# Kernel optimization log

Measured on AMD Instinct MI355X. Metric: run time of the kernel, lower is better.

## Reference

```python
import jax, jax.numpy as jnp
import numpy as np

T_VID = 129  # TACoS iou grid size

def make_iou_mask_map():
    m = np.zeros((129, 129), np.float32)
    for i in range(0, 128):
        m[i, 1 + i:min(i + 17, 129)] = 1.0
    for i in range(0, 128 - 16, 2):
        m[i, list(range(18 + i, min(33 + i, 129), 2))] = 1.0
    for i in range(0, 128 - 32, 4):
        m[i, list(range(36 + i, min(65 + i, 129), 4))] = 1.0
    for i in range(0, 128 - 64, 8):
        m[i, list(range(72 + i, 129, 8))] = 1.0
    return jnp.asarray(m)

def setup_inputs() -> dict:
    key = jax.random.key(0)
    B, L, T, D, CH, V = 8, 100, T_VID, 512, 512, 1000
    ks = jax.random.split(key, 20)
    g = lambda k, shp, fan: jax.random.normal(k, shp, jnp.float32) * (1.0 / np.sqrt(fan))
    return {
        'hidden_states_text': jax.random.normal(ks[0], (B, L, D), jnp.float32),
        'hidden_states_object': jax.random.normal(ks[1], (B, T, D), jnp.float32),
        # final_mlp (text head): D->CH->V
        'w_t1': g(ks[2], (D, CH), D), 'b_t1': jnp.zeros((CH,), jnp.float32),
        'w_t2': g(ks[3], (CH, V), CH), 'b_t2': jnp.zeros((V,), jnp.float32),
        # final_mlp_2: D -> 3D (+ReLU)
        'w2': g(ks[4], (D, 3 * D), D), 'b2': jnp.zeros((3 * D,), jnp.float32),
        # final_mlp_3: 3D -> CH -> 3
        'w3a': g(ks[5], (3 * D, CH), 3 * D), 'b3a': jnp.zeros((CH,), jnp.float32),
        'w3b': g(ks[6], (CH, 3), CH), 'b3b': jnp.zeros((3,), jnp.float32),
        # final_mlp_s/e/c: D -> CH -> 1
        'w_s1': g(ks[7], (D, CH), D), 'b_s1': jnp.zeros((CH,), jnp.float32),
        'w_s2': g(ks[8], (CH, 1), CH), 'b_s2': jnp.zeros((1,), jnp.float32),
        'w_e1': g(ks[9], (D, CH), D), 'b_e1': jnp.zeros((CH,), jnp.float32),
        'w_e2': g(ks[10], (CH, 1), CH), 'b_e2': jnp.zeros((1,), jnp.float32),
        'w_c1': g(ks[11], (D, CH), D), 'b_c1': jnp.zeros((CH,), jnp.float32),
        'w_c2': g(ks[12], (CH, 1), CH), 'b_c2': jnp.zeros((1,), jnp.float32),
    }

def _head(x, w1, b1, w2, b2):
    return jax.nn.relu(x @ w1 + b1) @ w2 + b2

def reference(hidden_states_text, hidden_states_object,
              w_t1, b_t1, w_t2, b_t2, w2, b2, w3a, b3a, w3b, b3b,
              w_s1, b_s1, w_s2, b_s2, w_e1, b_e1, w_e2, b_e2,
              w_c1, b_c1, w_c2, b_c2):
    D = hidden_states_object.shape[-1]
    T = hidden_states_object.shape[1]
    # text head (dropout is identity at inference)
    logits_text = _head(hidden_states_text, w_t1, b_t1, w_t2, b_t2)
    # final_mlp_2 then split into start/center/end streams, each [B,T,D]
    h = jax.nn.relu(hidden_states_object @ w2 + b2)
    hs, hc, he = h[..., :D], h[..., D:2 * D], h[..., 2 * D:]
    # final_mlp_3 first linear decomposed over the concat blocks:
    # grid[b,i,j] = W_s.hs[i] + W_c.hc[(i+j)//2] + W_e.he[j] + b  (same math as
    # cat(repeat(hs), gather(hc), repeat(he)) @ w3a, without the 3D grid)
    ps = hc @ w3a[D:2 * D]            # [B,T,CH] (center projection, gathered below)
    pS = hs @ w3a[:D]                 # [B,T,CH]
    pE = he @ w3a[2 * D:]             # [B,T,CH]
    idx = (jnp.arange(T)[:, None] + jnp.arange(T)[None, :]) // 2  # [T,T] center index
    grid = pS[:, :, None, :] + ps[:, idx, :] + pE[:, None, :, :] + b3a  # [B,T,T,CH]
    logits_iou = (jax.nn.relu(grid) @ w3b + b3b)  # [B,T,T,3]
    logits_iou = jnp.transpose(logits_iou, (0, 3, 1, 2))  # [B,3,T,T]
    logits_visual = jnp.concatenate([
        _head(hs, w_s1, b_s1, w_s2, b_s2),
        _head(he, w_e1, b_e1, w_e2, b_e2),
        _head(hc, w_c1, b_c1, w_c2, b_c2)], axis=-1)  # [B,T,3]
    return logits_text, logits_visual, logits_iou, make_iou_mask_map()
```

## Files before the change

### kernel.cpp

```cpp
#include <hip/hip_runtime.h>
#include <hip/hip_bf16.h>

typedef unsigned short ushort_t;
typedef __attribute__((ext_vector_type(8))) unsigned short u16x8;
typedef __attribute__((ext_vector_type(8))) short bf16x8;
typedef __attribute__((ext_vector_type(4))) float f32x4;

constexpr int BB = 8, LL = 100, TT = 129, DD = 512, CH = 512, VV = 1000;
constexpr int M_TXT = BB * LL;
constexpr int M_OBJ = BB * TT;
constexpr int P_SLAB = M_OBJ * DD;
constexpr int N_IOU = BB * 3 * TT * TT;
constexpr int N_VIS = 3 * M_OBJ;
constexpr int N_MASK = TT * TT;

constexpr int OUT_TEXT = 0;
constexpr int OUT_VIS  = M_TXT * VV;
constexpr int OUT_IOU  = OUT_VIS + N_VIS;
constexpr int OUT_MASK = OUT_IOU + N_IOU;

constexpr size_t WB_TEXT = 0;
constexpr size_t WB_OBJ  = WB_TEXT + 819200;
constexpr size_t WB_WT1  = WB_OBJ  + 1056768;
constexpr size_t WB_WT2  = WB_WT1  + 524288;
constexpr size_t WB_W2T  = WB_WT2  + 1024000;
constexpr size_t WB_W3AT = WB_W2T  + 1572864;
constexpr size_t WB_WS1T = WB_W3AT + 1572864;
constexpr size_t WB_WE1T = WB_WS1T + 524288;
constexpr size_t WB_WC1T = WB_WE1T + 524288;
constexpr size_t WB_T1   = WB_WC1T + 524288;
constexpr size_t WB_H    = WB_T1   + 819200;
constexpr size_t WB_P    = WB_H    + 3170304;

__device__ __forceinline__ ushort_t f2bf(float x) {
    __hip_bfloat16 h = __float2bfloat16(x);
    return *(ushort_t*)&h;
}

struct TDesc { const float* src; ushort_t* dst; int R, C, tiles, ctiles; };
struct PrepArgs {
    const float* act_a; ushort_t* act_da; int na4;
    const float* act_b; ushort_t* act_db; int nb4;
    int nact_blocks;
    TDesc t[7];
};

__global__ __launch_bounds__(256)
void prep_kernel(PrepArgs pa)
{
    const int bxg = blockIdx.x;
    if (bxg < pa.nact_blocks) {
        int gid = bxg * 256 + threadIdx.x;
        const float* src; ushort_t* dst;
        if (gid < pa.na4) { src = pa.act_a + gid * 4; dst = pa.act_da + gid * 4; }
        else { gid -= pa.na4; if (gid >= pa.nb4) return; src = pa.act_b + gid * 4; dst = pa.act_db + gid * 4; }
        f32x4 v = *(const f32x4*)src;
        dst[0] = f2bf(v[0]); dst[1] = f2bf(v[1]); dst[2] = f2bf(v[2]); dst[3] = f2bf(v[3]);
        return;
    }
    __shared__ float tl[32][65];
    int bx = bxg - pa.nact_blocks;
    TDesc e;
    #pragma unroll
    for (int i = 0; i < 7; ++i) {
        e = pa.t[i];
        if (bx < e.tiles) break;
        bx -= e.tiles;
    }
    const int t = threadIdx.x;
    const int rt = bx / e.ctiles, ct = bx - rt * e.ctiles;
    {
        const int c = t & 63, ty = t >> 6;
        const int gc = ct * 64 + c;
        const bool cok = gc < e.C;
        const float* sp = e.src + (size_t)(rt * 32) * e.C + gc;
        #pragma unroll
        for (int i = 0; i < 8; ++i) {
            const int rr = ty + i * 4;
            tl[rr][c] = cok ? sp[(size_t)rr * e.C] : 0.0f;
        }
    }
    __syncthreads();
    {
        const int dr = t >> 2, dc0 = (t & 3) << 3;
        const int gdr = ct * 64 + dr;
        if (gdr < e.C) {
            u16x8 v;
            #pragma unroll
            for (int u = 0; u < 8; ++u) v[u] = f2bf(tl[dc0 + u][dr]);
            *(u16x8*)&e.dst[(size_t)gdr * e.R + rt * 32 + dc0] = v;
        }
    }
}

struct GemmDesc {
    const ushort_t* A; int lda;
    const ushort_t* Bt; int ldb;
    const float* bias;
    void* C; int ldc;
    int M, N, K;
    int mode;
    const float* w2head;
    float* vbase;
    int vhead;
    int ntiles, ntx;
};
struct MegaArgs {
    GemmDesc d[7];
    int gemm_blocks;
    const float *b3b, *bs2, *be2, *bc2;
    float* out;
};

__global__ __launch_bounds__(256)
void mega_kernel(MegaArgs args)
{
    extern __shared__ char smem[];
    if ((int)blockIdx.x >= args.gemm_blocks) {
        int g = (blockIdx.x - args.gemm_blocks) * 1024 + threadIdx.x * 4;
        #pragma unroll
        for (int u = 0; u < 4; ++u, ++g) {
            int gg = g;
            if (gg < N_IOU) {
                const int bk = gg / (TT * TT);
                const int k = bk - (bk / 3) * 3;
                args.out[OUT_IOU + gg] = args.b3b[k];
                continue;
            }
            gg -= N_IOU;
            if (gg < N_VIS) {
                const int head = gg - (gg / 3) * 3;
                const float bias = head == 0 ? args.bs2[0] : (head == 1 ? args.be2[0] : args.bc2[0]);
                args.out[OUT_VIS + gg] = bias;
                continue;
            }
            gg -= N_VIS;
            if (gg < N_MASK) {
                const int i = gg / TT, j = gg - i * TT;
                const int d = j - i;
                bool v = false;
                if (i < 128 && d >= 1 && d <= 16) v = true;
                if (!v && (i & 1) == 0 && i <= 110 && d >= 18 && d <= 32 && (d & 1) == 0) v = true;
                if (!v && (i & 3) == 0 && i <= 92  && d >= 36 && d <= 64 && (d & 3) == 0) v = true;
                if (!v && (i & 7) == 0 && i <= 56  && d >= 72 && (d & 7) == 0) v = true;
                args.out[OUT_MASK + gg] = v ? 1.0f : 0.0f;
            }
        }
        return;
    }

    int bx = blockIdx.x, zi = 0;
    while (bx >= args.d[zi].ntiles) { bx -= args.d[zi].ntiles; ++zi; }
    const GemmDesc g = args.d[zi];
    const int tyT = bx / g.ntx, txT = bx - tyT * g.ntx;
    const int m0 = tyT * 128, n0 = txT * 128;

    ushort_t* ldsA = (ushort_t*)smem;
    ushort_t* ldsB = (ushort_t*)smem + 16384;

    const int tid = threadIdx.x;
    const int w = tid >> 6, l = tid & 63;
    const int wr = w >> 1, wc = w & 1;

    const int srow = l >> 2;
    const int scol = (l & 3) << 3;
    const int wbase = w << 4;

    f32x4 acc[4][4];
    #pragma unroll
    for (int mi = 0; mi < 4; ++mi)
        #pragma unroll
        for (int ni = 0; ni < 4; ++ni)
            acc[mi][ni] = f32x4{0.f, 0.f, 0.f, 0.f};

    const int nk = g.K >> 6;

    auto stage = [&](int buf, int k0) {
        #pragma unroll
        for (int ks = 0; ks < 2; ++ks) {
            const int sb = ((buf * 2 + ks) << 12);
            #pragma unroll
            for (int q = 0; q < 2; ++q) {
                int gm = m0 + (q << 6) + wbase + srow; if (gm >= g.M) gm = g.M - 1;
                __builtin_amdgcn_global_load_lds(
                    (const __attribute__((address_space(1))) unsigned int*)(g.A + (size_t)gm * g.lda + k0 + (ks << 5) + scol),
                    (__attribute__((address_space(3))) unsigned int*)(ldsA + sb + (((q << 6) + wbase) << 5)),
                    16, 0, 0);
                int gn = n0 + (q << 6) + wbase + srow; if (gn >= g.N) gn = g.N - 1;
                __builtin_amdgcn_global_load_lds(
                    (const __attribute__((address_space(1))) unsigned int*)(g.Bt + (size_t)gn * g.ldb + k0 + (ks << 5) + scol),
                    (__attribute__((address_space(3))) unsigned int*)(ldsB + sb + (((q << 6) + wbase) << 5)),
                    16, 0, 0);
            }
        }
    };

    stage(0, 0);
    int cur = 0;
    const int fr = l & 15, kq = (l >> 4) << 3;

    for (int kt = 0; kt < nk; ++kt) {
        __syncthreads();
        if (kt + 1 < nk) stage(cur ^ 1, (kt + 1) << 6);
        #pragma unroll
        for (int ks = 0; ks < 2; ++ks) {
            const int sb = ((cur * 2 + ks) << 12);
            bf16x8 av[4], bv[4];
            #pragma unroll
            for (int mi = 0; mi < 4; ++mi)
                av[mi] = *(const bf16x8*)(ldsA + sb + ((((wr << 6) + (mi << 4) + fr) << 5) + kq));
            #pragma unroll
            for (int ni = 0; ni < 4; ++ni)
                bv[ni] = *(const bf16x8*)(ldsB + sb + ((((wc << 6) + (ni << 4) + fr) << 5) + kq));
            #pragma unroll
            for (int mi = 0; mi < 4; ++mi)
                #pragma unroll
                for (int ni = 0; ni < 4; ++ni)
                    acc[mi][ni] = __builtin_amdgcn_mfma_f32_16x16x32_bf16(av[mi], bv[ni], acc[mi][ni], 0, 0, 0);
        }
        cur ^= 1;
    }

    const int rq = (l >> 4) << 2;
    if (g.mode == 2) {
        float s[4][4];
        #pragma unroll
        for (int mi = 0; mi < 4; ++mi)
            #pragma unroll
            for (int r = 0; r < 4; ++r) s[mi][r] = 0.f;
        #pragma unroll
        for (int ni = 0; ni < 4; ++ni) {
            const int col = n0 + (wc << 6) + (ni << 4) + fr;
            const float bb = g.bias[col];
            const float wv = g.w2head[col];
            #pragma unroll
            for (int mi = 0; mi < 4; ++mi)
                #pragma unroll
                for (int r = 0; r < 4; ++r) {
                    float v = fmaxf(acc[mi][ni][r] + bb, 0.f);
                    s[mi][r] = fmaf(v, wv, s[mi][r]);
                }
        }
        #pragma unroll
        for (int off = 1; off < 16; off <<= 1)
            #pragma unroll
            for (int mi = 0; mi < 4; ++mi)
                #pragma unroll
                for (int r = 0; r < 4; ++r)
                    s[mi][r] += __shfl_xor(s[mi][r], off);
        if (fr == 0) {
            #pragma unroll
            for (int mi = 0; mi < 4; ++mi)
                #pragma unroll
                for (int r = 0; r < 4; ++r) {
                    const int row = m0 + (wr << 6) + (mi << 4) + rq + r;
                    if (row < g.M) atomicAdd(&g.vbase[row * 3 + g.vhead], s[mi][r]);
                }
        }
    } else {
        #pragma unroll
        for (int ni = 0; ni < 4; ++ni) {
            const int col = n0 + (wc << 6) + (ni << 4) + fr;
            const float bb = (g.bias && col < g.N) ? g.bias[col] : 0.f;
            #pragma unroll
            for (int mi = 0; mi < 4; ++mi)
                #pragma unroll
                for (int r = 0; r < 4; ++r) {
                    const int row = m0 + (wr << 6) + (mi << 4) + rq + r;
                    if (row < g.M && col < g.N) {
                        float v = acc[mi][ni][r] + bb;
                        if (g.mode == 1) {
                            v = fmaxf(v, 0.f);
                            ((ushort_t*)g.C)[(size_t)row * g.ldc + col] = f2bf(v);
                        } else {
                            ((float*)g.C)[(size_t)row * g.ldc + col] = v;
                        }
                    }
                }
        }
    }
}

__global__ __launch_bounds__(256)
void iou_kernel(const float* __restrict__ P, const float* __restrict__ w3b,
                float* __restrict__ out)
{
    __shared__ __align__(16) float sP[96 * 132];
    __shared__ __align__(16) float sW[768];

    const int tid = threadIdx.x;
    const int b = blockIdx.z >> 1;
    const int half = blockIdx.z & 1;
    const int i0 = blockIdx.y * 32, j0 = blockIdx.x * 32;
    const int idx0 = (i0 + j0) >> 1;
    const int par = (i0 + j0) & 1;

    for (int f = tid; f < 768; f += 256) {
        const int ph = f / 384;
        const int rem = f - ph * 384;
        const int k = rem >> 7, c = rem & 127;
        sW[f] = w3b[((half << 8) + (ph << 7) + c) * 3 + k];
    }

    const int ii = tid >> 4, jj = tid & 15;
    const int o = ((ii + jj + par) >> 1) + 32;

    const f32x4 z4 = {0.f, 0.f, 0.f, 0.f};
    f32x4 av00[3], av01[3], av10[3], av11[3];
    #pragma unroll
    for (int k = 0; k < 3; ++k) { av00[k] = z4; av01[k] = z4; av10[k] = z4; av11[k] = z4; }

    for (int ph = 0; ph < 2; ++ph) {
        const int c0 = (half << 8) + (ph << 7);
        if (ph) __syncthreads();
        for (int f = tid; f < 3072; f += 256) {
            const int row = f >> 5;
            const int pos = (f & 31) << 2;
            const int a = row >> 5;
            const int r = row & 31;
            int rg = (a == 0) ? (i0 + r) : (a == 1) ? (idx0 + r) : (j0 + r);
            if (rg > 128) rg = 128;
            f32x4 v = *(const f32x4*)&P[(size_t)a * P_SLAB + ((size_t)(b * TT) + rg) * DD + c0 + pos];
            *(f32x4*)&sP[row * 132 + pos] = v;
        }
        __syncthreads();

        const float* rs0 = &sP[ii * 132];
        const float* rs1 = &sP[(ii + 16) * 132];
        const float* rp0 = &sP[o * 132];
        const float* rp1 = &sP[(o + 8) * 132];
        const float* rp2 = &sP[(o + 16) * 132];
        const float* re0 = &sP[(64 + jj) * 132];
        const float* re1 = &sP[(64 + jj + 16) * 132];
        const float* swp = &sW[ph * 384];

        #pragma unroll 2
        for (int c = 0; c < 128; c += 4) {
            const f32x4 s0 = *(const f32x4*)&rs0[c];
            const f32x4 s1 = *(const f32x4*)&rs1[c];
            const f32x4 p0 = *(const f32x4*)&rp0[c];
            const f32x4 p1 = *(const f32x4*)&rp1[c];
            const f32x4 p2 = *(const f32x4*)&rp2[c];
            const f32x4 e0 = *(const f32x4*)&re0[c];
            const f32x4 e1 = *(const f32x4*)&re1[c];
            const f32x4 w0 = *(const f32x4*)&swp[c];
            const f32x4 w1 = *(const f32x4*)&swp[128 + c];
            const f32x4 w2 = *(const f32x4*)&swp[256 + c];

            const f32x4 t00 = s0 + e0, t01 = s0 + e1, t10 = s1 + e0, t11 = s1 + e1;
            const f32x4 v00 = __builtin_elementwise_max(t00 + p0, z4);
            const f32x4 v01 = __builtin_elementwise_max(t01 + p1, z4);
            const f32x4 v10 = __builtin_elementwise_max(t10 + p1, z4);
            const f32x4 v11 = __builtin_elementwise_max(t11 + p2, z4);

            av00[0] = __builtin_elementwise_fma(v00, w0, av00[0]);
            av00[1] = __builtin_elementwise_fma(v00, w1, av00[1]);
            av00[2] = __builtin_elementwise_fma(v00, w2, av00[2]);
            av01[0] = __builtin_elementwise_fma(v01, w0, av01[0]);
            av01[1] = __builtin_elementwise_fma(v01, w1, av01[1]);
            av01[2] = __builtin_elementwise_fma(v01, w2, av01[2]);
            av10[0] = __builtin_elementwise_fma(v10, w0, av10[0]);
            av10[1] = __builtin_elementwise_fma(v10, w1, av10[1]);
            av10[2] = __builtin_elementwise_fma(v10, w2, av10[2]);
            av11[0] = __builtin_elementwise_fma(v11, w0, av11[0]);
            av11[1] = __builtin_elementwise_fma(v11, w1, av11[1]);
            av11[2] = __builtin_elementwise_fma(v11, w2, av11[2]);
        }
    }

    auto emit = [&](const f32x4* acc, int i, int j) {
        if (i <= 128 && j <= 128) {
            #pragma unroll
            for (int k = 0; k < 3; ++k) {
                const float s = acc[k][0] + acc[k][1] + acc[k][2] + acc[k][3];
                atomicAdd(&out[OUT_IOU + ((size_t)(b * 3 + k) * TT + i) * TT + j], s);
            }
        }
    };
    emit(av00, i0 + ii, j0 + jj);
    emit(av01, i0 + ii, j0 + jj + 16);
    emit(av10, i0 + ii + 16, j0 + jj);
    emit(av11, i0 + ii + 16, j0 + jj + 16);
}

extern "C" void kernel_launch(void* const* d_in, const int* in_sizes, int n_in,
                              void* d_out, int out_size, void* d_ws, size_t ws_size,
                              hipStream_t stream)
{
    const float* text = (const float*)d_in[0];
    const float* obj  = (const float*)d_in[1];
    const float* w_t1 = (const float*)d_in[2];
    const float* b_t1 = (const float*)d_in[3];
    const float* w_t2 = (const float*)d_in[4];
    const float* b_t2 = (const float*)d_in[5];
    const float* w2   = (const float*)d_in[6];
    const float* b2   = (const float*)d_in[7];
    const float* w3a  = (const float*)d_in[8];
    const float* b3a  = (const float*)d_in[9];
    const float* w3b  = (const float*)d_in[10];
    const float* b3b  = (const float*)d_in[11];
    const float* w_s1 = (const float*)d_in[12];
    const float* b_s1 = (const float*)d_in[13];
    const float* w_s2 = (const float*)d_in[14];
    const float* b_s2 = (const float*)d_in[15];
    const float* w_e1 = (const float*)d_in[16];
    const float* b_e1 = (const float*)d_in[17];
    const float* w_e2 = (const float*)d_in[18];
    const float* b_e2 = (const float*)d_in[19];
    const float* w_c1 = (const float*)d_in[20];
    const float* b_c1 = (const float*)d_in[21];
    const float* w_c2 = (const float*)d_in[22];
    const float* b_c2 = (const float*)d_in[23];

    float* out = (float*)d_out;
    char* ws = (char*)d_ws;
    ushort_t* text_bf = (ushort_t*)(ws + WB_TEXT);
    ushort_t* obj_bf  = (ushort_t*)(ws + WB_OBJ);
    ushort_t* wt1     = (ushort_t*)(ws + WB_WT1);
    ushort_t* wt2     = (ushort_t*)(ws + WB_WT2);
    ushort_t* w2t     = (ushort_t*)(ws + WB_W2T);
    ushort_t* w3at    = (ushort_t*)(ws + WB_W3AT);
    ushort_t* ws1t    = (ushort_t*)(ws + WB_WS1T);
    ushort_t* we1t    = (ushort_t*)(ws + WB_WE1T);
    ushort_t* wc1t    = (ushort_t*)(ws + WB_WC1T);
    ushort_t* T1      = (ushort_t*)(ws + WB_T1);
    ushort_t* H       = (ushort_t*)(ws + WB_H);
    float*    P       = (float*)(ws + WB_P);

    {
        PrepArgs pa;
        pa.act_a = text; pa.act_da = text_bf; pa.na4 = (M_TXT * DD) / 4;
        pa.act_b = obj;  pa.act_db = obj_bf;  pa.nb4 = (M_OBJ * DD) / 4;
        pa.nact_blocks = (pa.na4 + pa.nb4 + 255) / 256;
        pa.t[0] = {w_t1, wt1, 512, 512, 128, 8};
        pa.t[1] = {w_t2, wt2, 512, 1000, 256, 16};
        pa.t[2] = {w2, w2t, 512, 1536, 384, 24};
        pa.t[3] = {w3a, w3at, 1536, 512, 384, 8};
        pa.t[4] = {w_s1, ws1t, 512, 512, 128, 8};
        pa.t[5] = {w_e1, we1t, 512, 512, 128, 8};
        pa.t[6] = {w_c1, wc1t, 512, 512, 128, 8};
        prep_kernel<<<dim3(pa.nact_blocks + 1536), dim3(256), 0, stream>>>(pa);
    }
    {
        MegaArgs a{};
        a.d[0] = {text_bf, DD, wt1, DD, b_t1, T1, CH, M_TXT, CH, DD, 1, nullptr, nullptr, 0, 28, 4};
        a.d[1] = {obj_bf, DD, w2t, DD, b2, H, 3 * DD, M_OBJ, 3 * DD, DD, 1, nullptr, nullptr, 0, 108, 12};
        a.gemm_blocks = 136;
        a.b3b = b3b; a.bs2 = b_s2; a.be2 = b_e2; a.bc2 = b_c2; a.out = out;
        const int ninit = (N_IOU + N_VIS + N_MASK + 1023) / 1024;
        mega_kernel<<<dim3(136 + ninit), dim3(256), 65536, stream>>>(a);
    }
    {
        MegaArgs a{};
        a.d[0] = {T1, CH, wt2, CH, b_t2, out + OUT_TEXT, VV, M_TXT, VV, CH, 0, nullptr, nullptr, 0, 56, 8};
        a.d[1] = {H + 0 * DD, 3 * DD, w3at + 0 * DD, 3 * DD, b3a, P + 0 * P_SLAB, DD, M_OBJ, DD, DD, 0, nullptr, nullptr, 0, 36, 4};
        a.d[2] = {H + 1 * DD, 3 * DD, w3at + 1 * DD, 3 * DD, nullptr, P + 1 * P_SLAB, DD, M_OBJ, DD, DD, 0, nullptr, nullptr, 0, 36, 4};
        a.d[3] = {H + 2 * DD, 3 * DD, w3at + 2 * DD, 3 * DD, nullptr, P + 2 * P_SLAB, DD, M_OBJ, DD, DD, 0, nullptr, nullptr, 0, 36, 4};
        a.d[4] = {H + 0 * DD, 3 * DD, ws1t, DD, b_s1, nullptr, 0, M_OBJ, CH, DD, 2, w_s2, out + OUT_VIS, 0, 36, 4};
        a.d[5] = {H + 2 * DD, 3 * DD, we1t, DD, b_e1, nullptr, 0, M_OBJ, CH, DD, 2, w_e2, out + OUT_VIS, 1, 36, 4};
        a.d[6] = {H + 1 * DD, 3 * DD, wc1t, DD, b_c1, nullptr, 0, M_OBJ, CH, DD, 2, w_c2, out + OUT_VIS, 2, 36, 4};
        a.gemm_blocks = 272;
        a.b3b = b3b; a.bs2 = b_s2; a.be2 = b_e2; a.bc2 = b_c2; a.out = out;
        mega_kernel<<<dim3(272), dim3(256), 65536, stream>>>(a);
    }
    iou_kernel<<<dim3(5, 5, 16), dim3(256), 0, stream>>>(P, w3b, out);
}
```

Before: 76.96 us.

## Defer weight transposes into GEMM kernel and split IoU grid edge handling

Five weight transposes that the first GEMM stage does not need move out of the prep kernel and run as extra blocks of the first mega kernel, overlapping with the text and object GEMMs. The prep kernel therefore finishes sooner. The IoU kernel switches from a 5x5 tile grid, which wasted most of its last row and column of tiles on a single valid index, to 4x4 full tiles plus dedicated edge blocks that compute row 128 and column 128 with per-thread dot products. The bounds checks and clamping disappear from the main tiles, at the cost of a separate, less efficient edge path and more blocks in the first mega kernel.

```diff
diff --git a/kernel.cpp b/kernel.cpp
--- a/kernel.cpp
+++ b/kernel.cpp
@@ -13,6 +13,7 @@
 constexpr int N_IOU = BB * 3 * TT * TT;
 constexpr int N_VIS = 3 * M_OBJ;
 constexpr int N_MASK = TT * TT;
+constexpr int N_EDGE = BB * 257;
 
 constexpr int OUT_TEXT = 0;
 constexpr int OUT_VIS  = M_TXT * VV;
@@ -38,11 +39,39 @@
 }
 
 struct TDesc { const float* src; ushort_t* dst; int R, C, tiles, ctiles; };
+
+__device__ __forceinline__ void do_transpose_tile(const TDesc& e, int bx, int tid, float* tl )
+{
+    const int rt = bx / e.ctiles, ct = bx - rt * e.ctiles;
+    {
+        const int c = tid & 63, ty = tid >> 6;
+        const int gc = ct * 64 + c;
+        const bool cok = gc < e.C;
+        const float* sp = e.src + (size_t)(rt * 32) * e.C + gc;
+        #pragma unroll
+        for (int i = 0; i < 8; ++i) {
+            const int rr = ty + i * 4;
+            tl[rr * 65 + c] = cok ? sp[(size_t)rr * e.C] : 0.0f;
+        }
+    }
+    __syncthreads();
+    {
+        const int dr = tid >> 2, dc0 = (tid & 3) << 3;
+        const int gdr = ct * 64 + dr;
+        if (gdr < e.C) {
+            u16x8 v;
+            #pragma unroll
+            for (int u = 0; u < 8; ++u) v[u] = f2bf(tl[(dc0 + u) * 65 + dr]);
+            *(u16x8*)&e.dst[(size_t)gdr * e.R + rt * 32 + dc0] = v;
+        }
+    }
+}
+
 struct PrepArgs {
     const float* act_a; ushort_t* act_da; int na4;
     const float* act_b; ushort_t* act_db; int nb4;
     int nact_blocks;
-    TDesc t[7];
+    TDesc t[2];
 };
 
 __global__ __launch_bounds__(256)
@@ -58,39 +87,11 @@
         dst[0] = f2bf(v[0]); dst[1] = f2bf(v[1]); dst[2] = f2bf(v[2]); dst[3] = f2bf(v[3]);
         return;
     }
-    __shared__ float tl[32][65];
+    __shared__ float tl[32 * 65];
     int bx = bxg - pa.nact_blocks;
-    TDesc e;
-    #pragma unroll
-    for (int i = 0; i < 7; ++i) {
-        e = pa.t[i];
-        if (bx < e.tiles) break;
-        bx -= e.tiles;
-    }
-    const int t = threadIdx.x;
-    const int rt = bx / e.ctiles, ct = bx - rt * e.ctiles;
-    {
-        const int c = t & 63, ty = t >> 6;
-        const int gc = ct * 64 + c;
-        const bool cok = gc < e.C;
-        const float* sp = e.src + (size_t)(rt * 32) * e.C + gc;
-        #pragma unroll
-        for (int i = 0; i < 8; ++i) {
-            const int rr = ty + i * 4;
-            tl[rr][c] = cok ? sp[(size_t)rr * e.C] : 0.0f;
-        }
-    }
-    __syncthreads();
-    {
-        const int dr = t >> 2, dc0 = (t & 3) << 3;
-        const int gdr = ct * 64 + dr;
-        if (gdr < e.C) {
-            u16x8 v;
-            #pragma unroll
-            for (int u = 0; u < 8; ++u) v[u] = f2bf(tl[dc0 + u][dr]);
-            *(u16x8*)&e.dst[(size_t)gdr * e.R + rt * 32 + dc0] = v;
-        }
-    }
+    TDesc e = pa.t[0];
+    if (bx >= e.tiles) { bx -= e.tiles; e = pa.t[1]; }
+    do_transpose_tile(e, bx, threadIdx.x, tl);
 }
 
 struct GemmDesc {
@@ -108,6 +109,8 @@
 struct MegaArgs {
     GemmDesc d[7];
     int gemm_blocks;
+    TDesc t[5];
+    int wt_blocks;
     const float *b3b, *bs2, *be2, *bc2;
     float* out;
 };
@@ -117,7 +120,19 @@
 {
     extern __shared__ char smem[];
     if ((int)blockIdx.x >= args.gemm_blocks) {
-        int g = (blockIdx.x - args.gemm_blocks) * 1024 + threadIdx.x * 4;
+        int wx = blockIdx.x - args.gemm_blocks;
+        if (wx < args.wt_blocks) {
+            TDesc e;
+            #pragma unroll
+            for (int i = 0; i < 5; ++i) {
+                e = args.t[i];
+                if (wx < e.tiles) break;
+                wx -= e.tiles;
+            }
+            do_transpose_tile(e, wx, threadIdx.x, (float*)smem);
+            return;
+        }
+        int g = (wx - args.wt_blocks) * 1024 + threadIdx.x * 4;
         #pragma unroll
         for (int u = 0; u < 4; ++u, ++g) {
             int gg = g;
@@ -289,11 +304,54 @@
     __shared__ __align__(16) float sW[768];
 
     const int tid = threadIdx.x;
-    const int b = blockIdx.z >> 1;
-    const int half = blockIdx.z & 1;
-    const int i0 = blockIdx.y * 32, j0 = blockIdx.x * 32;
+    const int bxg = blockIdx.x;
+
+    if (bxg >= 256) {
+        for (int f = tid; f < 1536; f += 256) {
+            const int k = f >> 9, c = f & 511;
+            sP[f] = w3b[c * 3 + k];
+        }
+        __syncthreads();
+        const int pt = (bxg - 256) * 64 + (tid >> 2);
+        if (pt >= N_EDGE) return;
+        const int b = pt / 257;
+        const int r = pt - b * 257;
+        int i, j;
+        if (r < 129) { i = 128; j = r; } else { i = r - 129; j = 128; }
+        const int idx = (i + j) >> 1;
+        const int c0 = (tid & 3) << 7;
+
+        const float* rs = P + ((size_t)(b * TT) + i) * DD + c0;
+        const float* rp = P + (size_t)P_SLAB + ((size_t)(b * TT) + idx) * DD + c0;
+        const float* re = P + (size_t)2 * P_SLAB + ((size_t)(b * TT) + j) * DD + c0;
+        const float* w0 = &sP[c0], *w1 = &sP[512 + c0], *w2 = &sP[1024 + c0];
+
+        float a0 = 0.f, a1 = 0.f, a2 = 0.f;
+        for (int c = 0; c < 128; c += 4) {
+            const f32x4 s = *(const f32x4*)&rs[c];
+            const f32x4 p = *(const f32x4*)&rp[c];
+            const f32x4 e = *(const f32x4*)&re[c];
+            #pragma unroll
+            for (int u = 0; u < 4; ++u) {
+                const float v = fmaxf(s[u] + p[u] + e[u], 0.f);
+                a0 = fmaf(v, w0[c + u], a0);
+                a1 = fmaf(v, w1[c + u], a1);
+                a2 = fmaf(v, w2[c + u], a2);
+            }
+        }
+        const size_t base = ((size_t)(b * 3) * TT + i) * TT + j;
+        atomicAdd(&out[OUT_IOU + base], a0);
+        atomicAdd(&out[OUT_IOU + base + TT * TT], a1);
+        atomicAdd(&out[OUT_IOU + base + 2 * TT * TT], a2);
+        return;
+    }
+
+    const int half = bxg & 1;
+    const int b = (bxg >> 1) & 7;
+    const int tj = (bxg >> 4) & 3;
+    const int ti = (bxg >> 6) & 3;
+    const int i0 = ti * 32, j0 = tj * 32;
     const int idx0 = (i0 + j0) >> 1;
-    const int par = (i0 + j0) & 1;
 
     for (int f = tid; f < 768; f += 256) {
         const int ph = f / 384;
@@ -303,7 +361,7 @@
     }
 
     const int ii = tid >> 4, jj = tid & 15;
-    const int o = ((ii + jj + par) >> 1) + 32;
+    const int o = ((ii + jj) >> 1) + 32;
 
     const f32x4 z4 = {0.f, 0.f, 0.f, 0.f};
     f32x4 av00[3], av01[3], av10[3], av11[3];
@@ -317,9 +375,8 @@
             const int row = f >> 5;
             const int pos = (f & 31) << 2;
             const int a = row >> 5;
-            const int r = row & 31;
-            int rg = (a == 0) ? (i0 + r) : (a == 1) ? (idx0 + r) : (j0 + r);
-            if (rg > 128) rg = 128;
+            const int rr = row & 31;
+            const int rg = (a == 0) ? (i0 + rr) : (a == 1) ? (idx0 + rr) : (j0 + rr);
             f32x4 v = *(const f32x4*)&P[(size_t)a * P_SLAB + ((size_t)(b * TT) + rg) * DD + c0 + pos];
             *(f32x4*)&sP[row * 132 + pos] = v;
         }
@@ -369,12 +426,10 @@
     }
 
     auto emit = [&](const f32x4* acc, int i, int j) {
-        if (i <= 128 && j <= 128) {
-            #pragma unroll
-            for (int k = 0; k < 3; ++k) {
-                const float s = acc[k][0] + acc[k][1] + acc[k][2] + acc[k][3];
-                atomicAdd(&out[OUT_IOU + ((size_t)(b * 3 + k) * TT + i) * TT + j], s);
-            }
+        #pragma unroll
+        for (int k = 0; k < 3; ++k) {
+            const float s = acc[k][0] + acc[k][1] + acc[k][2] + acc[k][3];
+            atomicAdd(&out[OUT_IOU + ((size_t)(b * 3 + k) * TT + i) * TT + j], s);
         }
     };
     emit(av00, i0 + ii, j0 + jj);
@@ -433,22 +488,23 @@
         pa.act_b = obj;  pa.act_db = obj_bf;  pa.nb4 = (M_OBJ * DD) / 4;
         pa.nact_blocks = (pa.na4 + pa.nb4 + 255) / 256;
         pa.t[0] = {w_t1, wt1, 512, 512, 128, 8};
-        pa.t[1] = {w_t2, wt2, 512, 1000, 256, 16};
-        pa.t[2] = {w2, w2t, 512, 1536, 384, 24};
-        pa.t[3] = {w3a, w3at, 1536, 512, 384, 8};
-        pa.t[4] = {w_s1, ws1t, 512, 512, 128, 8};
-        pa.t[5] = {w_e1, we1t, 512, 512, 128, 8};
-        pa.t[6] = {w_c1, wc1t, 512, 512, 128, 8};
-        prep_kernel<<<dim3(pa.nact_blocks + 1536), dim3(256), 0, stream>>>(pa);
+        pa.t[1] = {w2, w2t, 512, 1536, 384, 24};
+        prep_kernel<<<dim3(pa.nact_blocks + 512), dim3(256), 0, stream>>>(pa);
     }
     {
         MegaArgs a{};
         a.d[0] = {text_bf, DD, wt1, DD, b_t1, T1, CH, M_TXT, CH, DD, 1, nullptr, nullptr, 0, 28, 4};
         a.d[1] = {obj_bf, DD, w2t, DD, b2, H, 3 * DD, M_OBJ, 3 * DD, DD, 1, nullptr, nullptr, 0, 108, 12};
         a.gemm_blocks = 136;
+        a.t[0] = {w_t2, wt2, 512, 1000, 256, 16};
+        a.t[1] = {w3a, w3at, 1536, 512, 384, 8};
+        a.t[2] = {w_s1, ws1t, 512, 512, 128, 8};
+        a.t[3] = {w_e1, we1t, 512, 512, 128, 8};
+        a.t[4] = {w_c1, wc1t, 512, 512, 128, 8};
+        a.wt_blocks = 1024;
         a.b3b = b3b; a.bs2 = b_s2; a.be2 = b_e2; a.bc2 = b_c2; a.out = out;
         const int ninit = (N_IOU + N_VIS + N_MASK + 1023) / 1024;
-        mega_kernel<<<dim3(136 + ninit), dim3(256), 65536, stream>>>(a);
+        mega_kernel<<<dim3(136 + 1024 + ninit), dim3(256), 65536, stream>>>(a);
     }
     {
         MegaArgs a{};
@@ -460,8 +516,9 @@
         a.d[5] = {H + 2 * DD, 3 * DD, we1t, DD, b_e1, nullptr, 0, M_OBJ, CH, DD, 2, w_e2, out + OUT_VIS, 1, 36, 4};
         a.d[6] = {H + 1 * DD, 3 * DD, wc1t, DD, b_c1, nullptr, 0, M_OBJ, CH, DD, 2, w_c2, out + OUT_VIS, 2, 36, 4};
         a.gemm_blocks = 272;
+        a.wt_blocks = 0;
         a.b3b = b3b; a.bs2 = b_s2; a.be2 = b_e2; a.bc2 = b_c2; a.out = out;
         mega_kernel<<<dim3(272), dim3(256), 65536, stream>>>(a);
     }
-    iou_kernel<<<dim3(5, 5, 16), dim3(256), 0, stream>>>(P, w3b, out);
+    iou_kernel<<<dim3(256 + (N_EDGE + 63) / 64), dim3(256), 0, stream>>>(P, w3b, out);
 }
```

New measurement: 77.14 us. About the same (+0.2%).
